# Optimization experiments

Hardware: AMD Instinct MI355X
Metric: run time of the kernel (lower is better)

The kernel has to match this reference:

```python
import jax, jax.numpy as jnp
import numpy as np

N, E, D = 100000, 1600000, 128      # nodes, edges, in_channels = MLP out_dim
L = 3                               # num GIN layers
OC = D + L * D                      # concat width = 512
CH, CHID = 4, 256                   # num ChannelMLPs, their hidden dim


def setup_inputs() -> dict:
    key = jax.random.key(0)
    ks = jax.random.split(key, 10)
    s = lambda fan_in: 1.0 / np.sqrt(fan_in)
    x = jax.random.normal(ks[0], (N, D), dtype=jnp.float32)
    edge_index = jax.random.randint(ks[1], (2, E), 0, N, dtype=jnp.int32)
    # conv MLPs: per layer 3 linear layers (in->hid, hid->hid, hid->out), all 128x128
    convW = jax.random.normal(ks[2], (L, 3, D, D), dtype=jnp.float32) * s(D)
    convB = jnp.zeros((L, 3, D), dtype=jnp.float32)
    # channel MLPs: 512 -> 256 -> 256 -> 1, ReLU after every layer (output_activation='relu')
    chanW1 = jax.random.normal(ks[3], (CH, OC, CHID), dtype=jnp.float32) * s(OC)
    chanB1 = jnp.zeros((CH, CHID), dtype=jnp.float32)
    chanW2 = jax.random.normal(ks[4], (CH, CHID, CHID), dtype=jnp.float32) * s(CHID)
    chanB2 = jnp.zeros((CH, CHID), dtype=jnp.float32)
    chanW3 = jax.random.normal(ks[5], (CH, CHID, 1), dtype=jnp.float32) * s(CHID)
    chanB3 = jnp.zeros((CH, 1), dtype=jnp.float32)
    return {"x": x, "edge_index": edge_index, "convW": convW, "convB": convB,
            "chanW1": chanW1, "chanB1": chanB1, "chanW2": chanW2, "chanB2": chanB2,
            "chanW3": chanW3, "chanB3": chanB3}


def reference(x, edge_index, convW, convB, chanW1, chanB1, chanW2, chanB2, chanW3, chanB3):
    src, dst = edge_index[0], edge_index[1]
    n = x.shape[0]
    feats = [x]                      # skip_first_features=False -> keep input
    h = x
    for l in range(L):
        # GINConv, eps=0: mlp((1+eps)*h + sum_{j in N(i)} h_j)
        agg = jax.ops.segment_sum(h[src], dst, num_segments=n)  # scatter-add at targets
        h = h + agg
        for k in range(3):           # MLP: Lin+ReLU x3 (2 hidden + relu output activation)
            h = jax.nn.relu(h @ convW[l, k] + convB[l, k])
        feats.append(h)
    xcat = jnp.concatenate(feats, axis=1)                       # [N, 512]
    # channel MLPs vectorized over the channel axis c
    h1 = jax.nn.relu(jnp.einsum('nd,cdh->cnh', xcat, chanW1) + chanB1[:, None, :])
    h2 = jax.nn.relu(jnp.einsum('cnh,chk->cnk', h1, chanW2) + chanB2[:, None, :])
    h3 = jax.nn.relu(jnp.einsum('cnh,cho->cno', h2, chanW3) + chanB3[:, None, :])
    return jnp.transpose(h3[..., 0])                            # [N, num_ChannelMLPs]
```

## Files before the change

### kernel.cpp

```cpp
#include <hip/hip_runtime.h>
#include <hip/hip_bf16.h>

#define D 128
#define NLAYER 3
#define NCH 4

typedef __attribute__((ext_vector_type(8))) short short8;
typedef __attribute__((ext_vector_type(4))) float f32x4;

__device__ __forceinline__ ushort f2bf(float f) {
    unsigned int u = __builtin_bit_cast(unsigned int, f);
    u += 0x7fffu + ((u >> 16) & 1u);
    return (ushort)(u >> 16);
}
__device__ __forceinline__ float bflo(unsigned int u) {
    return __builtin_bit_cast(float, u << 16);
}
__device__ __forceinline__ float bfhi(unsigned int u) {
    return __builtin_bit_cast(float, u & 0xffff0000u);
}

#define FILL_CHUNK 4096
__global__ __launch_bounds__(256) void hist_part_kernel(
    const int* __restrict__ dst, int* __restrict__ deg,
    int E, int nPer, int N)
{
    int cls = blockIdx.x & 7;
    int base = (blockIdx.x >> 3) * FILL_CHUNK;
    int lo = cls * nPer;
    int hi = lo + nPer; if (hi > N) hi = N;
    int end = base + FILL_CHUNK; if (end > E) end = E;
    for (int e = base + threadIdx.x; e < end; e += 256) {
        int d = dst[e];
        if (d >= lo && d < hi) atomicAdd(&deg[d], 1);
    }
}

__global__ __launch_bounds__(256) void blocksum_kernel(
    const int* __restrict__ deg, int* __restrict__ bsum, int n)
{
    int i = blockIdx.x * 256 + threadIdx.x;
    int v = (i < n) ? deg[i] : 0;
#pragma unroll
    for (int o = 1; o < 64; o <<= 1) v += __shfl_xor(v, o);
    __shared__ int s[4];
    if ((threadIdx.x & 63) == 0) s[threadIdx.x >> 6] = v;
    __syncthreads();
    if (threadIdx.x == 0) bsum[blockIdx.x] = s[0] + s[1] + s[2] + s[3];
}

__global__ __launch_bounds__(512) void scanblk_kernel(
    const int* __restrict__ bsum, int* __restrict__ boff, int nb,
    int* __restrict__ offs, int n, int E)
{
    __shared__ int sh[512];
    int t = threadIdx.x;
    sh[t] = (t < nb) ? bsum[t] : 0;
    __syncthreads();
    for (int d = 1; d < 512; d <<= 1) {
        int v = (t >= d) ? sh[t - d] : 0;
        __syncthreads();
        sh[t] += v;
        __syncthreads();
    }
    if (t < nb) boff[t] = (t == 0) ? 0 : sh[t - 1];
    if (t == 0) offs[n] = E;
}

__global__ __launch_bounds__(256) void blockscan_kernel(
    const int* __restrict__ deg, const int* __restrict__ boff,
    int* __restrict__ offs, int* __restrict__ cursor, int n)
{
    __shared__ int sh[256];
    int t = threadIdx.x;
    int i = blockIdx.x * 256 + t;
    int v = (i < n) ? deg[i] : 0;
    sh[t] = v;
    __syncthreads();
    for (int d = 1; d < 256; d <<= 1) {
        int u = (t >= d) ? sh[t - d] : 0;
        __syncthreads();
        sh[t] += u;
        __syncthreads();
    }
    if (i < n) {
        int ex = boff[blockIdx.x] + sh[t] - v;
        offs[i] = ex; cursor[i] = ex;
    }
}

__global__ __launch_bounds__(256) void fill_part_kernel(
    const int* __restrict__ src, const int* __restrict__ dst,
    int* __restrict__ cursor, int* __restrict__ csr,
    int E, int nPer, int N)
{
    int cls = blockIdx.x & 7;
    int base = (blockIdx.x >> 3) * FILL_CHUNK;
    int lo = cls * nPer;
    int hi = lo + nPer; if (hi > N) hi = N;
    int end = base + FILL_CHUNK; if (end > E) end = E;
    for (int e = base + threadIdx.x; e < end; e += 256) {
        int d = dst[e];
        int s = src[e];
        if (d >= lo && d < hi) {
            int p = atomicAdd(&cursor[d], 1);
            csr[p] = s;
        }
    }
}

__global__ __launch_bounds__(256) void cvtx_kernel(
    const float* __restrict__ x, ushort* __restrict__ xb, int total8)
{
    int i = blockIdx.x * 256 + threadIdx.x;
    if (i >= total8) return;
    const float* gp = x + (size_t)i * 8;
    float4 v0 = *(const float4*)gp;
    float4 v1 = *(const float4*)(gp + 4);
    short8 pk;
    pk[0] = (short)f2bf(v0.x); pk[1] = (short)f2bf(v0.y);
    pk[2] = (short)f2bf(v0.z); pk[3] = (short)f2bf(v0.w);
    pk[4] = (short)f2bf(v1.x); pk[5] = (short)f2bf(v1.y);
    pk[6] = (short)f2bf(v1.z); pk[7] = (short)f2bf(v1.w);
    *(short8*)(xb + (size_t)i * 8) = pk;
}

__global__ void cvtW_kernel(const float* __restrict__ W, ushort* __restrict__ Wt,
                            int K, int Ncols) {
    __shared__ float tile[32][33];
    int c = blockIdx.z;
    int k0 = blockIdx.x * 32, n0 = blockIdx.y * 32;
    const float* Wc = W + (size_t)c * K * Ncols;
    ushort* Wtc = Wt + (size_t)c * K * Ncols;
    int tx = threadIdx.x & 31, ty = threadIdx.x >> 5;
#pragma unroll
    for (int i = 0; i < 4; ++i) {
        int k = k0 + ty + i * 8;
        tile[ty + i * 8][tx] = Wc[(size_t)k * Ncols + n0 + tx];
    }
    __syncthreads();
#pragma unroll
    for (int i = 0; i < 4; ++i) {
        int n = n0 + ty + i * 8;
        Wtc[(size_t)n * K + k0 + tx] = f2bf(tile[tx][ty + i * 8]);
    }
}

__global__ __launch_bounds__(256) void agg_bf16(
    const ushort* __restrict__ h,
    const int* __restrict__ offs, const int* __restrict__ csr,
    ushort* __restrict__ outb, int n)
{
    int node = (blockIdx.x * 256 + threadIdx.x) >> 4;
    int l16 = threadIdx.x & 15;
    if (node >= n) return;
    uint4 u = *((const uint4*)(h + (size_t)node * 128) + l16);
    float a0 = bflo(u.x), a1 = bfhi(u.x);
    float a2 = bflo(u.y), a3 = bfhi(u.y);
    float a4 = bflo(u.z), a5 = bfhi(u.z);
    float a6 = bflo(u.w), a7 = bfhi(u.w);
    int b = offs[node], e = offs[node + 1];
    int j = b;

#define ACC4(v0, v1, v2, v3)                                         \
    do {                                                             \
        a0 += (bflo(v0.x) + bflo(v1.x)) + (bflo(v2.x) + bflo(v3.x)); \
        a1 += (bfhi(v0.x) + bfhi(v1.x)) + (bfhi(v2.x) + bfhi(v3.x)); \
        a2 += (bflo(v0.y) + bflo(v1.y)) + (bflo(v2.y) + bflo(v3.y)); \
        a3 += (bfhi(v0.y) + bfhi(v1.y)) + (bfhi(v2.y) + bfhi(v3.y)); \
        a4 += (bflo(v0.z) + bflo(v1.z)) + (bflo(v2.z) + bflo(v3.z)); \
        a5 += (bfhi(v0.z) + bfhi(v1.z)) + (bfhi(v2.z) + bfhi(v3.z)); \
        a6 += (bflo(v0.w) + bflo(v1.w)) + (bflo(v2.w) + bflo(v3.w)); \
        a7 += (bfhi(v0.w) + bfhi(v1.w)) + (bfhi(v2.w) + bfhi(v3.w)); \
    } while (0)

    if (j + 4 <= e) {
        int i0 = csr[j], i1 = csr[j + 1], i2 = csr[j + 2], i3 = csr[j + 3];
        uint4 v0 = *((const uint4*)(h + (size_t)i0 * 128) + l16);
        uint4 v1 = *((const uint4*)(h + (size_t)i1 * 128) + l16);
        uint4 v2 = *((const uint4*)(h + (size_t)i2 * 128) + l16);
        uint4 v3 = *((const uint4*)(h + (size_t)i3 * 128) + l16);
        j += 4;
        int p0 = 0, p1 = 0, p2 = 0, p3 = 0;
        bool have = (j + 4 <= e);
        if (have) { p0 = csr[j]; p1 = csr[j + 1]; p2 = csr[j + 2]; p3 = csr[j + 3]; }
        while (have) {
            uint4 w0 = *((const uint4*)(h + (size_t)p0 * 128) + l16);
            uint4 w1 = *((const uint4*)(h + (size_t)p1 * 128) + l16);
            uint4 w2 = *((const uint4*)(h + (size_t)p2 * 128) + l16);
            uint4 w3 = *((const uint4*)(h + (size_t)p3 * 128) + l16);
            int nj = j + 4;
            bool nxt = (nj + 4 <= e);
            if (nxt) { p0 = csr[nj]; p1 = csr[nj + 1]; p2 = csr[nj + 2]; p3 = csr[nj + 3]; }
            ACC4(v0, v1, v2, v3);
            v0 = w0; v1 = w1; v2 = w2; v3 = w3;
            j = nj; have = nxt;
        }
        ACC4(v0, v1, v2, v3);
    }
    for (; j < e; ++j) {
        uint4 v0 = *((const uint4*)(h + (size_t)csr[j] * 128) + l16);
        a0 += bflo(v0.x); a1 += bfhi(v0.x);
        a2 += bflo(v0.y); a3 += bfhi(v0.y);
        a4 += bflo(v0.z); a5 += bfhi(v0.z);
        a6 += bflo(v0.w); a7 += bfhi(v0.w);
    }
#undef ACC4
    uint4 po;
    po.x = (unsigned int)f2bf(a0) | ((unsigned int)f2bf(a1) << 16);
    po.y = (unsigned int)f2bf(a2) | ((unsigned int)f2bf(a3) << 16);
    po.z = (unsigned int)f2bf(a4) | ((unsigned int)f2bf(a5) << 16);
    po.w = (unsigned int)f2bf(a6) | ((unsigned int)f2bf(a7) << 16);
    *((uint4*)(outb + (size_t)node * 128) + l16) = po;
}

__global__ __launch_bounds__(256) void gin_mlp_mfma(
    const ushort* __restrict__ A,
    const ushort* __restrict__ WtL,
    const float* __restrict__ biasL,
    ushort* __restrict__ Out,
    int nrows)
{
    __shared__ __align__(16) ushort As[128 * 128];
    __shared__ __align__(16) ushort Bs[128 * 128];
    const int t = threadIdx.x;
    const int w = t >> 6, lane = t & 63;
    const int quad = lane >> 4, c15 = lane & 15;
    const int wr = w >> 1, wc = w & 1;
    const int rowbase = blockIdx.x * 128;

#pragma unroll
    for (int i = 0; i < 8; ++i) {
        int lin = (i * 4 + w) * 64 + lane;
        int row = lin >> 4, slot = lin & 15, g = slot ^ (row & 15);
        int grow = rowbase + row;
        if (grow >= nrows) grow = 0;
        const ushort* gp = A + (size_t)grow * 128 + g * 8;
        __builtin_amdgcn_global_load_lds(
            (const __attribute__((address_space(1))) void*)gp,
            (__attribute__((address_space(3))) void*)&As[(i * 4 + w) * 512],
            16, 0, 0);
    }
#pragma unroll
    for (int i = 0; i < 8; ++i) {
        int lin = (i * 4 + w) * 64 + lane;
        int n = lin >> 4, slot = lin & 15, g = slot ^ (n & 15);
        const ushort* gp = WtL + (size_t)n * 128 + g * 8;
        __builtin_amdgcn_global_load_lds(
            (const __attribute__((address_space(1))) void*)gp,
            (__attribute__((address_space(3))) void*)&Bs[(i * 4 + w) * 512],
            16, 0, 0);
    }
    __syncthreads();

    for (int s = 0; s < 3; ++s) {
        f32x4 acc[4][4];
#pragma unroll
        for (int i = 0; i < 4; ++i)
#pragma unroll
            for (int j = 0; j < 4; ++j)
#pragma unroll
                for (int r = 0; r < 4; ++r) acc[i][j][r] = 0.f;

#pragma unroll
        for (int ks = 0; ks < 4; ++ks) {
            short8 af[4], bf[4];
#pragma unroll
            for (int tr = 0; tr < 4; ++tr) {
                int r = wr * 64 + tr * 16 + c15;
                af[tr] = *(const short8*)&As[r * 128 + (((ks * 4 + quad) ^ (r & 15)) * 8)];
            }
#pragma unroll
            for (int tc = 0; tc < 4; ++tc) {
                int n = wc * 64 + tc * 16 + c15;
                bf[tc] = *(const short8*)&Bs[n * 128 + (((ks * 4 + quad) ^ (n & 15)) * 8)];
            }
#pragma unroll
            for (int tr = 0; tr < 4; ++tr)
#pragma unroll
                for (int tc = 0; tc < 4; ++tc)
                    acc[tr][tc] = __builtin_amdgcn_mfma_f32_16x16x32_bf16(
                        af[tr], bf[tc], acc[tr][tc], 0, 0, 0);
        }
        __syncthreads();

        if (s < 2) {
#pragma unroll
            for (int tc = 0; tc < 4; ++tc) {
                int col = wc * 64 + tc * 16 + c15;
                float bv = biasL[s * 128 + col];
#pragma unroll
                for (int tr = 0; tr < 4; ++tr)
#pragma unroll
                    for (int rg = 0; rg < 4; ++rg) {
                        int row = wr * 64 + tr * 16 + quad * 4 + rg;
                        As[row * 128 + (((col >> 3) ^ (row & 15)) * 8) + (col & 7)]
                            = f2bf(fmaxf(acc[tr][tc][rg] + bv, 0.f));
                    }
            }
            const ushort* Wn = WtL + (size_t)(s + 1) * 128 * 128;
#pragma unroll
            for (int i = 0; i < 8; ++i) {
                int lin = (i * 4 + w) * 64 + lane;
                int n = lin >> 4, slot = lin & 15, g = slot ^ (n & 15);
                const ushort* gp = Wn + (size_t)n * 128 + g * 8;
                __builtin_amdgcn_global_load_lds(
                    (const __attribute__((address_space(1))) void*)gp,
                    (__attribute__((address_space(3))) void*)&Bs[(i * 4 + w) * 512],
                    16, 0, 0);
            }
            __syncthreads();
        } else {
#pragma unroll
            for (int tc = 0; tc < 4; ++tc) {
                int col = wc * 64 + tc * 16 + c15;
                float bv = biasL[2 * 128 + col];
#pragma unroll
                for (int tr = 0; tr < 4; ++tr)
#pragma unroll
                    for (int rg = 0; rg < 4; ++rg) {
                        int grow = rowbase + wr * 64 + tr * 16 + quad * 4 + rg;
                        if (grow < nrows)
                            Out[(size_t)grow * 128 + col]
                                = f2bf(fmaxf(acc[tr][tc][rg] + bv, 0.f));
                    }
            }
        }
    }
}

__global__ __launch_bounds__(256, 2) void chan_fused_mfma(
    const ushort* __restrict__ A0, const ushort* __restrict__ A1,
    const ushort* __restrict__ A2, const ushort* __restrict__ A3,
    const ushort* __restrict__ Wt1,
    const float* __restrict__ b1,
    const ushort* __restrict__ Wt2,
    const float* __restrict__ b2,
    const float* __restrict__ w3,
    const float* __restrict__ b3,
    float* __restrict__ out,
    int N, int T, int chunkT)
{
    const int bid = blockIdx.x;
    const int xcd = bid & 7;
    const int idx = bid >> 3;
    const int c = idx & 3;
    const int rt = xcd * chunkT + (idx >> 2);
    if (rt >= T) return;
    const int rowbase = rt * 64;

    __shared__ __align__(16) ushort As2[2][64 * 64];
    __shared__ __align__(16) ushort Bs2[2][256 * 64];
    ushort* Ts = &Bs2[1][0];
    float (*red)[4] = (float (*)[4]) & As2[0][0];

    const int t = threadIdx.x;
    const int w = t >> 6, lane = t & 63;
    const int quad = lane >> 4, c15 = lane & 15;
    const ushort* W1c = Wt1 + (size_t)c * 256 * 512;
    const ushort* W2c = Wt2 + (size_t)c * 256 * 256;

    int a_grow[2], a_g[2];
#pragma unroll
    for (int i = 0; i < 2; ++i) {
        int lin = (i * 4 + w) * 64 + lane;
        int row = lin >> 3, slot = lin & 7;
        a_g[i] = slot ^ (row & 7);
        int g = rowbase + row;
        a_grow[i] = (g < N) ? g : 0;
    }
    auto stageA = [&](int buf, int kc) {
        int ai = kc >> 7;
        const ushort* Ab = (ai == 0) ? A0 : (ai == 1) ? A1 : (ai == 2) ? A2 : A3;
        const int within = kc & 127;
#pragma unroll
        for (int i = 0; i < 2; ++i) {
            const ushort* gp = Ab + (size_t)a_grow[i] * 128 + within + a_g[i] * 8;
            __builtin_amdgcn_global_load_lds(
                (const __attribute__((address_space(1))) void*)gp,
                (__attribute__((address_space(3))) void*)&As2[buf][(i * 4 + w) * 512],
                16, 0, 0);
        }
    };
    int b_n[8], b_g[8];
#pragma unroll
    for (int i = 0; i < 8; ++i) {
        int lin = (i * 4 + w) * 64 + lane;
        b_n[i] = lin >> 3;
        b_g[i] = (lin & 7) ^ (b_n[i] & 7);
    }
    auto stageB = [&](int buf, const ushort* Wn, int ldk, int kc) {
#pragma unroll
        for (int i = 0; i < 8; ++i) {
            const ushort* gp = Wn + (size_t)b_n[i] * ldk + kc + b_g[i] * 8;
            __builtin_amdgcn_global_load_lds(
                (const __attribute__((address_space(1))) void*)gp,
                (__attribute__((address_space(3))) void*)&Bs2[buf][(i * 4 + w) * 512],
                16, 0, 0);
        }
    };

    f32x4 acc[4][4];
#pragma unroll
    for (int i = 0; i < 4; ++i)
#pragma unroll
        for (int j = 0; j < 4; ++j)
#pragma unroll
            for (int r = 0; r < 4; ++r) acc[i][j][r] = 0.f;

    stageA(1, 0);
    stageB(1, W1c, 512, 0);
#pragma unroll
    for (int s = 0; s < 8; ++s) {
        const int cur = (s + 1) & 1;
        if (s < 7) {
            stageA(cur ^ 1, (s + 1) * 64);
            stageB(cur ^ 1, W1c, 512, (s + 1) * 64);
            asm volatile("s_waitcnt vmcnt(10)" ::: "memory");
        } else {
            asm volatile("s_waitcnt vmcnt(0)" ::: "memory");
        }
        __builtin_amdgcn_s_barrier();
        __builtin_amdgcn_sched_barrier(0);
#pragma unroll
        for (int ks = 0; ks < 2; ++ks) {
            short8 af[4], bf[4];
#pragma unroll
            for (int tr = 0; tr < 4; ++tr) {
                int r = tr * 16 + c15;
                af[tr] = *(const short8*)&As2[cur][r * 64 + (((ks * 4 + quad) ^ (r & 7)) * 8)];
            }
#pragma unroll
            for (int tc = 0; tc < 4; ++tc) {
                int n = w * 64 + tc * 16 + c15;
                bf[tc] = *(const short8*)&Bs2[cur][n * 64 + (((ks * 4 + quad) ^ (n & 7)) * 8)];
            }
#pragma unroll
            for (int tr = 0; tr < 4; ++tr)
#pragma unroll
                for (int tc = 0; tc < 4; ++tc)
                    acc[tr][tc] = __builtin_amdgcn_mfma_f32_16x16x32_bf16(
                        af[tr], bf[tc], acc[tr][tc], 0, 0, 0);
        }
        __builtin_amdgcn_s_barrier();
    }

    stageB(0, W2c, 256, 0);
#pragma unroll
    for (int tc = 0; tc < 4; ++tc) {
        int col = w * 64 + tc * 16 + c15;
        float bv = b1[c * 256 + col];
#pragma unroll
        for (int tr = 0; tr < 4; ++tr)
#pragma unroll
            for (int rg = 0; rg < 4; ++rg) {
                int row = tr * 16 + quad * 4 + rg;
                Ts[row * 256 + (((col >> 3) ^ (row & 31)) * 8) + (col & 7)]
                    = f2bf(fmaxf(acc[tr][tc][rg] + bv, 0.f));
            }
    }
    __syncthreads();

#pragma unroll
    for (int i = 0; i < 4; ++i)
#pragma unroll
        for (int j = 0; j < 4; ++j)
#pragma unroll
            for (int r = 0; r < 4; ++r) acc[i][j][r] = 0.f;

#pragma unroll
    for (int s = 0; s < 4; ++s) {
#pragma unroll
        for (int ks = 0; ks < 2; ++ks) {
            short8 af[4], bf[4];
            const int g0 = s * 8 + ks * 4 + quad;
#pragma unroll
            for (int tr = 0; tr < 4; ++tr) {
                int r = tr * 16 + c15;
                af[tr] = *(const short8*)&Ts[r * 256 + ((g0 ^ (r & 31)) * 8)];
            }
#pragma unroll
            for (int tc = 0; tc < 4; ++tc) {
                int n = w * 64 + tc * 16 + c15;
                bf[tc] = *(const short8*)&Bs2[0][n * 64 + (((ks * 4 + quad) ^ (n & 7)) * 8)];
            }
#pragma unroll
            for (int tr = 0; tr < 4; ++tr)
#pragma unroll
                for (int tc = 0; tc < 4; ++tc)
                    acc[tr][tc] = __builtin_amdgcn_mfma_f32_16x16x32_bf16(
                        af[tr], bf[tc], acc[tr][tc], 0, 0, 0);
        }
        if (s < 3) {
            __syncthreads();
            stageB(0, W2c, 256, (s + 1) * 64);
            __syncthreads();
        }
    }

    float b2v[4], w3v[4];
#pragma unroll
    for (int tc = 0; tc < 4; ++tc) {
        int col = w * 64 + tc * 16 + c15;
        b2v[tc] = b2[c * 256 + col];
        w3v[tc] = w3[c * 256 + col];
    }
    __syncthreads();
#pragma unroll
    for (int tr = 0; tr < 4; ++tr)
#pragma unroll
        for (int rg = 0; rg < 4; ++rg) {
            float p = 0.f;
#pragma unroll
            for (int tc = 0; tc < 4; ++tc)
                p += fmaxf(acc[tr][tc][rg] + b2v[tc], 0.f) * w3v[tc];
            p += __shfl_xor(p, 1);
            p += __shfl_xor(p, 2);
            p += __shfl_xor(p, 4);
            p += __shfl_xor(p, 8);
            if (c15 == 0) red[tr * 16 + quad * 4 + rg][w] = p;
        }
    __syncthreads();
    if (t < 64) {
        int grow = rowbase + t;
        if (grow < N) {
            float s = red[t][0] + red[t][1] + red[t][2] + red[t][3] + b3[c];
            out[(size_t)grow * NCH + c] = fmaxf(s, 0.f);
        }
    }
}

extern "C" void kernel_launch(void* const* d_in, const int* in_sizes, int n_in,
                              void* d_out, int out_size, void* d_ws, size_t ws_size,
                              hipStream_t stream) {
    const float* x        = (const float*)d_in[0];
    const int*   eidx     = (const int*)d_in[1];
    const float* convW    = (const float*)d_in[2];
    const float* convB    = (const float*)d_in[3];
    const float* chanW1   = (const float*)d_in[4];
    const float* chanB1   = (const float*)d_in[5];
    const float* chanW2   = (const float*)d_in[6];
    const float* chanB2   = (const float*)d_in[7];
    const float* chanW3   = (const float*)d_in[8];
    const float* chanB3   = (const float*)d_in[9];
    float* out = (float*)d_out;

    const int N = in_sizes[0] / D;
    const int E = in_sizes[1] / 2;
    const int* srcp = eidx;
    const int* dstp = eidx + E;
    const int nb = (N + 255) / 256;

    char* w = (char*)d_ws;
    auto take = [&](size_t bytes) {
        char* p = w;
        w += (bytes + 255) & ~(size_t)255;
        return p;
    };
    ushort* xb     = (ushort*)take((size_t)N * D * 2);
    ushort* h0     = (ushort*)take((size_t)N * D * 2);
    ushort* h1     = (ushort*)take((size_t)N * D * 2);
    ushort* h2     = (ushort*)take((size_t)N * D * 2);
    int*    deg    = (int*)take((size_t)N * 4);
    int*    offs   = (int*)take((size_t)(N + 1) * 4);
    int*    cursor = (int*)take((size_t)N * 4);
    int*    bsum   = (int*)take((size_t)nb * 4);
    int*    boff   = (int*)take((size_t)nb * 4);
    ushort* Wt1b   = (ushort*)take((size_t)NCH * 256 * 512 * 2);
    ushort* Wt2b   = (ushort*)take((size_t)NCH * 256 * 256 * 2);
    ushort* WtC    = (ushort*)take((size_t)NLAYER * 3 * D * D * 2);

    size_t used = (size_t)(w - (char*)d_ws);
    if (used > ws_size) return;
    size_t rem = ws_size - used;
    size_t need_gin = (((size_t)E * 4 + 255) & ~(size_t)255) + (size_t)N * D * 2;
    if (rem < need_gin) return;

    int*    csr = (int*)w;
    ushort* a   = (ushort*)(w + (((size_t)E * 4 + 255) & ~(size_t)255));

    hipMemsetAsync(deg, 0, (size_t)N * 4, stream);
    {
        int nchunks = (E + FILL_CHUNK - 1) / FILL_CHUNK;
        int nPer = (N + 7) / 8;
        hist_part_kernel<<<nchunks * 8, 256, 0, stream>>>(dstp, deg, E, nPer, N);
        blocksum_kernel<<<nb, 256, 0, stream>>>(deg, bsum, N);
        scanblk_kernel<<<1, 512, 0, stream>>>(bsum, boff, nb, offs, N, E);
        blockscan_kernel<<<nb, 256, 0, stream>>>(deg, boff, offs, cursor, N);
        fill_part_kernel<<<nchunks * 8, 256, 0, stream>>>(
            srcp, dstp, cursor, csr, E, nPer, N);
    }

    cvtx_kernel<<<(N * 16 + 255) / 256, 256, 0, stream>>>(x, xb, N * 16);
    cvtW_kernel<<<dim3(512 / 32, 256 / 32, NCH), 256, 0, stream>>>(chanW1, Wt1b, 512, 256);
    cvtW_kernel<<<dim3(256 / 32, 256 / 32, NCH), 256, 0, stream>>>(chanW2, Wt2b, 256, 256);
    cvtW_kernel<<<dim3(D / 32, D / 32, NLAYER * 3), 256, 0, stream>>>(convW, WtC, D, D);

    const int rowtiles = (N + 127) / 128;
    const int aggblocks = (N * 16 + 255) / 256;

    ushort* hbuf[NLAYER] = {h0, h1, h2};
    const ushort* prev = xb;
    for (int l = 0; l < NLAYER; ++l) {
        agg_bf16<<<aggblocks, 256, 0, stream>>>(prev, offs, csr, a, N);
        gin_mlp_mfma<<<rowtiles, 256, 0, stream>>>(
            a, WtC + (size_t)l * 3 * D * D, convB + (size_t)l * 3 * D, hbuf[l], N);
        prev = hbuf[l];
    }

    {
        const int T = (N + 63) / 64;
        const int chunkT = (T + 7) / 8;
        const int grid = 8 * chunkT * NCH;
        chan_fused_mfma<<<grid, 256, 0, stream>>>(
            xb, h0, h1, h2,
            Wt1b, chanB1, Wt2b, chanB2, chanW3, chanB3,
            out, N, T, chunkT);
    }
}
```

Before: 816.3 us.

## Sort nodes by degree so aggregation waves process similar-degree nodes

Builds a degree histogram, a descending scan and a scatter to produce a permutation of nodes ordered by in-degree. The aggregation kernel then processes nodes in that order, so the 16-lane groups within a wavefront have similar edge counts and waste fewer idle lanes. It adds three small preprocessing kernels plus an indirection load per node, and adjacent groups now read scattered node rows instead of contiguous ones.

```diff
diff --git a/kernel.cpp b/kernel.cpp
--- a/kernel.cpp
+++ b/kernel.cpp
@@ -109,6 +109,50 @@
     }
 }
 
+#define DBINS 512
+__global__ __launch_bounds__(256) void deghist_kernel(
+    const int* __restrict__ deg, int* __restrict__ dhist, int n)
+{
+    __shared__ int lh[DBINS];
+    int t = threadIdx.x;
+    lh[t] = 0; lh[t + 256] = 0;
+    __syncthreads();
+    for (int i = blockIdx.x * 256 + t; i < n; i += gridDim.x * 256) {
+        int d = deg[i]; if (d > DBINS - 1) d = DBINS - 1;
+        atomicAdd(&lh[d], 1);
+    }
+    __syncthreads();
+    if (lh[t]) atomicAdd(&dhist[t], lh[t]);
+    if (lh[t + 256]) atomicAdd(&dhist[t + 256], lh[t + 256]);
+}
+
+__global__ __launch_bounds__(DBINS) void degscan_kernel(
+    const int* __restrict__ dhist, int* __restrict__ dcur)
+{
+    __shared__ int sh[DBINS];
+    int t = threadIdx.x;
+    sh[t] = dhist[DBINS - 1 - t];
+    __syncthreads();
+    for (int d = 1; d < DBINS; d <<= 1) {
+        int v = (t >= d) ? sh[t - d] : 0;
+        __syncthreads();
+        sh[t] += v;
+        __syncthreads();
+    }
+    dcur[DBINS - 1 - t] = sh[t] - dhist[DBINS - 1 - t];
+}
+
+__global__ __launch_bounds__(256) void degscatter_kernel(
+    const int* __restrict__ deg, int* __restrict__ dcur,
+    int* __restrict__ perm, int n)
+{
+    int i = blockIdx.x * 256 + threadIdx.x;
+    if (i >= n) return;
+    int d = deg[i]; if (d > DBINS - 1) d = DBINS - 1;
+    int pos = atomicAdd(&dcur[d], 1);
+    perm[pos] = i;
+}
+
 __global__ __launch_bounds__(256) void cvtx_kernel(
     const float* __restrict__ x, ushort* __restrict__ xb, int total8)
 {
@@ -149,11 +193,13 @@
 __global__ __launch_bounds__(256) void agg_bf16(
     const ushort* __restrict__ h,
     const int* __restrict__ offs, const int* __restrict__ csr,
+    const int* __restrict__ perm,
     ushort* __restrict__ outb, int n)
 {
-    int node = (blockIdx.x * 256 + threadIdx.x) >> 4;
+    int qw = (blockIdx.x * 256 + threadIdx.x) >> 4;
     int l16 = threadIdx.x & 15;
-    if (node >= n) return;
+    if (qw >= n) return;
+    int node = perm[qw];
     uint4 u = *((const uint4*)(h + (size_t)node * 128) + l16);
     float a0 = bflo(u.x), a1 = bfhi(u.x);
     float a2 = bflo(u.y), a3 = bfhi(u.y);
@@ -566,6 +612,9 @@
     int*    cursor = (int*)take((size_t)N * 4);
     int*    bsum   = (int*)take((size_t)nb * 4);
     int*    boff   = (int*)take((size_t)nb * 4);
+    int*    dhist  = (int*)take((size_t)DBINS * 4);
+    int*    dcur   = (int*)take((size_t)DBINS * 4);
+    int*    perm   = (int*)take((size_t)N * 4);
     ushort* Wt1b   = (ushort*)take((size_t)NCH * 256 * 512 * 2);
     ushort* Wt2b   = (ushort*)take((size_t)NCH * 256 * 256 * 2);
     ushort* WtC    = (ushort*)take((size_t)NLAYER * 3 * D * D * 2);
@@ -580,6 +629,7 @@
     ushort* a   = (ushort*)(w + (((size_t)E * 4 + 255) & ~(size_t)255));
 
     hipMemsetAsync(deg, 0, (size_t)N * 4, stream);
+    hipMemsetAsync(dhist, 0, (size_t)DBINS * 4, stream);
     {
         int nchunks = (E + FILL_CHUNK - 1) / FILL_CHUNK;
         int nPer = (N + 7) / 8;
@@ -589,6 +639,9 @@
         blockscan_kernel<<<nb, 256, 0, stream>>>(deg, boff, offs, cursor, N);
         fill_part_kernel<<<nchunks * 8, 256, 0, stream>>>(
             srcp, dstp, cursor, csr, E, nPer, N);
+        deghist_kernel<<<64, 256, 0, stream>>>(deg, dhist, N);
+        degscan_kernel<<<1, DBINS, 0, stream>>>(dhist, dcur);
+        degscatter_kernel<<<nb, 256, 0, stream>>>(deg, dcur, perm, N);
     }
 
     cvtx_kernel<<<(N * 16 + 255) / 256, 256, 0, stream>>>(x, xb, N * 16);
@@ -602,7 +655,7 @@
     ushort* hbuf[NLAYER] = {h0, h1, h2};
     const ushort* prev = xb;
     for (int l = 0; l < NLAYER; ++l) {
-        agg_bf16<<<aggblocks, 256, 0, stream>>>(prev, offs, csr, a, N);
+        agg_bf16<<<aggblocks, 256, 0, stream>>>(prev, offs, csr, perm, a, N);
         gin_mlp_mfma<<<rowtiles, 256, 0, stream>>>(
             a, WtC + (size_t)l * 3 * D * D, convB + (size_t)l * 3 * D, hbuf[l], N);
         prev = hbuf[l];
```

New measurement: 1.100 ms. 34.8% more time.
